# Performance work log

Measured on AMD Instinct MI355X. Metric: run time of the kernel, lower is better.

The kernel has to match this reference:

```python
import jax, jax.numpy as jnp
import numpy as np

N_NODES = 50000


def gin_conv(x, src, dst, W, b, eps=0.0):
    # GINConv: nn((1+eps)*x_i + sum_{j in N(i)} x_j)
    agg = jax.ops.segment_sum(x[src], dst, num_segments=N_NODES)  # [N, D]
    h = (1.0 + eps) * x + agg
    return h @ W + b


def setup_inputs() -> dict:
    key = jax.random.key(0)
    ks = jax.random.split(key, 8)
    n, e = N_NODES, 800000
    d_in, d_h, d_out = 128, 128, 64
    feature = jax.random.normal(ks[0], (n, d_in), dtype=jnp.float32)
    edge_index = jax.random.randint(ks[1], (2, e), 0, n, dtype=jnp.int64)
    s1 = 1.0 / np.sqrt(d_in)
    sh = 1.0 / np.sqrt(d_h)
    W1 = jax.random.normal(ks[2], (d_in, d_h), dtype=jnp.float32) * s1
    b1 = jnp.zeros((d_h,), dtype=jnp.float32)
    Wh = jax.random.normal(ks[3], (d_h, d_h), dtype=jnp.float32) * sh
    bh = jnp.zeros((d_h,), dtype=jnp.float32)
    Wo = jax.random.normal(ks[4], (d_h, d_out), dtype=jnp.float32) * sh
    bo = jnp.zeros((d_out,), dtype=jnp.float32)
    return {"feature": feature, "edge_index": edge_index, "W1": W1, "b1": b1,
            "Wh": Wh, "bh": bh, "Wo": Wo, "bo": bo}


def reference(feature, edge_index, W1, b1, Wh, bh, Wo, bo):
    src, dst = edge_index[0], edge_index[1]
    x = gin_conv(feature, src, dst, W1, b1)
    x = jax.nn.relu(x)
    # one hidden layer (layer_num=3); dropout disabled (eval)
    x = gin_conv(x, src, dst, Wh, bh)
    x = jax.nn.relu(x)
    x = gin_conv(x, src, dst, Wo, bo)
    return jax.nn.log_softmax(x, axis=1)
```

## Files before the change

### kernel.cpp

```cpp
#include <hip/hip_runtime.h>

typedef short short8 __attribute__((ext_vector_type(8)));
typedef float f32x4 __attribute__((ext_vector_type(4)));


__device__ inline unsigned short f2bf(float f) {
    union { float f; unsigned u; } v; v.f = f;
    unsigned r = v.u + 0x7fffu + ((v.u >> 16) & 1u);
    return (unsigned short)(r >> 16);
}
__device__ inline unsigned pack2(float a, float b) {
    return (unsigned)f2bf(a) | ((unsigned)f2bf(b) << 16);
}
__device__ inline float bflo(unsigned u) { union { unsigned q; float f; } c; c.q = u << 16; return c.f; }
__device__ inline float bfhi(unsigned u) { union { unsigned q; float f; } c; c.q = u & 0xffff0000u; return c.f; }


#define EPB 2048
#define NE 8
#define BSH 9
#define MAXBKT 128
#define DCAP 10240

__global__ __launch_bounds__(256) void binA(const int* __restrict__ src, const int* __restrict__ dst,
                                            int* __restrict__ cnt2d, int e, int nbkt, int nblk) {
    __shared__ int hist[MAXBKT];
    int t = threadIdx.x, blk = blockIdx.x;
    for (int b = t; b < nbkt; b += 256) hist[b] = 0;
    __syncthreads();
    int base = blk * EPB;
#pragma unroll
    for (int j = 0; j < NE; j++) {
        int idx = base + t + 256 * j;
        if (idx < e) atomicAdd(&hist[dst[idx] >> BSH], 1);
    }
    __syncthreads();
    for (int b = t; b < nbkt; b += 256) cnt2d[b * nblk + blk] = hist[b];
}

__global__ __launch_bounds__(512) void scanB1(int* __restrict__ cnt2d, int* __restrict__ totals, int nblk) {
    __shared__ int s[512];
    int t = threadIdx.x, b = blockIdx.x;
    int v = (t < nblk) ? cnt2d[b * nblk + t] : 0;
    s[t] = v;
    __syncthreads();
    for (int off = 1; off < 512; off <<= 1) {
        int u = (t >= off) ? s[t - off] : 0;
        __syncthreads();
        s[t] += u;
        __syncthreads();
    }
    if (t < nblk) cnt2d[b * nblk + t] = s[t] - v;
    if (t == nblk - 1) totals[b] = s[t];
}

__global__ __launch_bounds__(128) void scanB2(const int* __restrict__ totals, int* __restrict__ bbase,
                                              int* __restrict__ row_ptr, int nbkt, int n, int e) {
    __shared__ int s[128];
    int t = threadIdx.x;
    int v = (t < nbkt) ? totals[t] : 0;
    s[t] = v;
    __syncthreads();
    for (int off = 1; off < 128; off <<= 1) {
        int u = (t >= off) ? s[t - off] : 0;
        __syncthreads();
        s[t] += u;
        __syncthreads();
    }
    if (t < nbkt) bbase[t] = s[t] - v;
    if (t == 0) row_ptr[n] = e;
}

__global__ __launch_bounds__(256) void binC(const int* __restrict__ src, const int* __restrict__ dst,
                                            const int* __restrict__ cnt2d, const int* __restrict__ bbase,
                                            unsigned* __restrict__ pairs, int e, int nbkt, int nblk) {
    __shared__ int hist[MAXBKT], loff[MAXBKT], cur[MAXBKT], gb[MAXBKT];
    __shared__ int sc[256];
    __shared__ unsigned sorted[EPB];
    int t = threadIdx.x, blk = blockIdx.x;
    for (int b = t; b < nbkt; b += 256) hist[b] = 0;
    __syncthreads();
    int base = blk * EPB;
    int cnt = min(EPB, e - base);
    unsigned packed[NE];
    int bb[NE];
#pragma unroll
    for (int j = 0; j < NE; j++) {
        int idx = base + t + 256 * j;
        bb[j] = -1;
        if (idx < e) {
            unsigned s0 = (unsigned)src[idx], d = (unsigned)dst[idx];
            int b = (int)(d >> BSH);
            bb[j] = b;
            packed[j] = s0 | ((d & ((1u << BSH) - 1)) << 16) | ((unsigned)b << 25);
            atomicAdd(&hist[b], 1);
        }
    }
    __syncthreads();
    int v = (t < nbkt) ? hist[t] : 0;
    sc[t] = v;
    __syncthreads();
    for (int off = 1; off < 256; off <<= 1) {
        int u = (t >= off) ? sc[t - off] : 0;
        __syncthreads();
        sc[t] += u;
        __syncthreads();
    }
    if (t < nbkt) {
        int ex = sc[t] - v;
        loff[t] = ex;
        cur[t] = ex;
        gb[t] = bbase[t] + cnt2d[t * nblk + blk];
    }
    __syncthreads();
#pragma unroll
    for (int j = 0; j < NE; j++) {
        if (bb[j] >= 0) {
            int r = atomicAdd(&cur[bb[j]], 1);
            sorted[r] = packed[j];
        }
    }
    __syncthreads();
    for (int i = t; i < cnt; i += 256) {
        unsigned w = sorted[i];
        int b = (int)(w >> 25);
        pairs[gb[b] + (i - loff[b])] = w;
    }
}

__global__ __launch_bounds__(512) void buildD(const unsigned* __restrict__ pairs,
                                              const int* __restrict__ totals, const int* __restrict__ bbase,
                                              int* __restrict__ row_ptr, unsigned short* __restrict__ csr, int n) {
    __shared__ int hist[512], off[512];
    __shared__ unsigned short lcsr[DCAP];
    int t = threadIdx.x, b = blockIdx.x;
    int cnt = totals[b], base = bbase[b];
    hist[t] = 0;
    __syncthreads();
    for (int i = t; i < cnt; i += 512)
        atomicAdd(&hist[(pairs[base + i] >> 16) & 511], 1);
    __syncthreads();
    int v = hist[t];
    off[t] = v;
    __syncthreads();
    for (int o = 1; o < 512; o <<= 1) {
        int u = (t >= o) ? off[t - o] : 0;
        __syncthreads();
        off[t] += u;
        __syncthreads();
    }
    int excl = off[t] - v;
    int node = (b << BSH) + t;
    if (node < n) row_ptr[node] = base + excl;
    __syncthreads();
    hist[t] = excl;
    __syncthreads();
    for (int i = t; i < cnt; i += 512) {
        unsigned w = pairs[base + i];
        int r = atomicAdd(&hist[(w >> 16) & 511], 1);
        if (r < DCAP) lcsr[r] = (unsigned short)(w & 0xFFFFu);
    }
    __syncthreads();
    int lim = min(cnt, DCAP);
    for (int i = t; i < lim; i += 512) csr[base + i] = lcsr[i];
}


__global__ void cvt_bf16_kernel(const float4* __restrict__ in, uint2* __restrict__ out, int nf4) {
    int i = blockIdx.x * 256 + threadIdx.x;
    if (i < nf4) {
        float4 v = in[i];
        out[i] = make_uint2(pack2(v.x, v.y), pack2(v.z, v.w));
    }
}

__global__ void wt_all(const float* __restrict__ W1, const float* __restrict__ Wh, const float* __restrict__ Wo,
                       unsigned short* __restrict__ W1t, unsigned short* __restrict__ Wht,
                       unsigned short* __restrict__ Wot) {
    int i = blockIdx.x * 256 + threadIdx.x;
    if (i < 16384) {
        int k = i >> 7, nn = i & 127;
        W1t[nn * 128 + k] = f2bf(W1[i]);
    } else if (i < 32768) {
        int j = i - 16384, k = j >> 7, nn = j & 127;
        Wht[nn * 128 + k] = f2bf(Wh[j]);
    } else if (i < 40960) {
        int j = i - 32768, k = j >> 6, nn = j & 63;
        Wot[nn * 128 + k] = f2bf(Wo[j]);
    }
}


#define ACC8(vv)                                     \
    acc[0] += bflo(vv.x); acc[1] += bfhi(vv.x);      \
    acc[2] += bflo(vv.y); acc[3] += bfhi(vv.y);      \
    acc[4] += bflo(vv.z); acc[5] += bfhi(vv.z);      \
    acc[6] += bflo(vv.w); acc[7] += bfhi(vv.w);


template <bool SECOND>
__global__ __launch_bounds__(256) void fused_layer(
    const uint4* __restrict__ x, const int* __restrict__ row_ptr,
    const unsigned short* __restrict__ csr,
    const short8* __restrict__ Bt, const float* __restrict__ bias,
    unsigned short* __restrict__ out_h,
    const short8* __restrict__ Bt2,
    unsigned short* __restrict__ out_y,
    int n) {
    __shared__ unsigned short As[16][136];
    __shared__ unsigned short Hs[SECOND ? 16 : 1][SECOND ? 136 : 1];

    int t = threadIdx.x;
    int nl = t >> 4, chunk = t & 15;
    int r0 = blockIdx.x * 16;
    int node = r0 + nl;

    float acc[8] = {0.f, 0.f, 0.f, 0.f, 0.f, 0.f, 0.f, 0.f};
    if (node < n) {
        size_t base = (size_t)node * 16 + chunk;
        uint4 s0 = x[base];
        ACC8(s0)
        int beg = row_ptr[node], end = row_ptr[node + 1];
        int ed = beg;
        for (; ed + 8 <= end; ed += 8) {
            int idx[8];
#pragma unroll
            for (int j = 0; j < 8; j++) idx[j] = csr[ed + j];
            uint4 v[8];
#pragma unroll
            for (int j = 0; j < 8; j++) v[j] = x[(size_t)idx[j] * 16 + chunk];
#pragma unroll
            for (int j = 0; j < 8; j++) { ACC8(v[j]) }
        }
        for (; ed + 4 <= end; ed += 4) {
            int i0 = csr[ed], i1 = csr[ed + 1], i2 = csr[ed + 2], i3 = csr[ed + 3];
            uint4 v0 = x[(size_t)i0 * 16 + chunk];
            uint4 v1 = x[(size_t)i1 * 16 + chunk];
            uint4 v2 = x[(size_t)i2 * 16 + chunk];
            uint4 v3 = x[(size_t)i3 * 16 + chunk];
            ACC8(v0) ACC8(v1) ACC8(v2) ACC8(v3)
        }
        for (; ed < end; ++ed) {
            uint4 v0 = x[(size_t)csr[ed] * 16 + chunk];
            ACC8(v0)
        }
    }
    uint4 packed;
    packed.x = pack2(acc[0], acc[1]); packed.y = pack2(acc[2], acc[3]);
    packed.z = pack2(acc[4], acc[5]); packed.w = pack2(acc[6], acc[7]);
    ((uint4*)&As[nl][0])[chunk] = packed;
    __syncthreads();

    int wid = t >> 6, lane = t & 63;
    int lm = lane & 15, lq = lane >> 4;

    short8 a[4];
#pragma unroll
    for (int kc = 0; kc < 4; kc++)
        a[kc] = *(const short8*)&As[lm][kc * 32 + lq * 8];

    f32x4 hacc[2];
#pragma unroll
    for (int nt = 0; nt < 2; nt++) hacc[nt] = (f32x4){0.f, 0.f, 0.f, 0.f};
#pragma unroll
    for (int nt = 0; nt < 2; nt++) {
        int ct = wid * 2 + nt;
        const short8* Br = Bt + (size_t)(ct * 16 + lm) * 16;
#pragma unroll
        for (int kc = 0; kc < 4; kc++)
            hacc[nt] = __builtin_amdgcn_mfma_f32_16x16x32_bf16(a[kc], Br[kc * 4 + lq], hacc[nt], 0, 0, 0);
    }

#pragma unroll
    for (int nt = 0; nt < 2; nt++) {
        int col = (wid * 2 + nt) * 16 + lm;
        float bv = bias[col];
#pragma unroll
        for (int i = 0; i < 4; i++) {
            int row = r0 + lq * 4 + i;
            float v = fmaxf(hacc[nt][i] + bv, 0.f);
            if (SECOND) {
                Hs[lq * 4 + i][col] = f2bf(v);
            } else if (row < n) {
                out_h[(size_t)row * 128 + col] = f2bf(v);
            }
        }
    }

    if (SECOND) {
        __syncthreads();
        short8 a2[4];
#pragma unroll
        for (int kc = 0; kc < 4; kc++)
            a2[kc] = *(const short8*)&Hs[lm][kc * 32 + lq * 8];
        f32x4 yacc = (f32x4){0.f, 0.f, 0.f, 0.f};
        const short8* Br2 = Bt2 + (size_t)(wid * 16 + lm) * 16;
#pragma unroll
        for (int kc = 0; kc < 4; kc++)
            yacc = __builtin_amdgcn_mfma_f32_16x16x32_bf16(a2[kc], Br2[kc * 4 + lq], yacc, 0, 0, 0);
        int col = wid * 16 + lm;
#pragma unroll
        for (int i = 0; i < 4; i++) {
            int row = r0 + lq * 4 + i;
            if (row < n) out_y[(size_t)row * 64 + col] = f2bf(yacc[i]);
        }
    }
}


__global__ __launch_bounds__(256) void agg_lsm(
    const uint4* __restrict__ x, float* __restrict__ out,
    const int* __restrict__ row_ptr, const unsigned short* __restrict__ csr,
    const float* __restrict__ bo, int n) {
    int gt = blockIdx.x * 256 + threadIdx.x;
    int node = gt >> 3, lane = gt & 7;
    if (node >= n) return;
    size_t base = (size_t)node * 8 + lane;
    uint4 s0 = x[base];
    float acc[8] = { bflo(s0.x), bfhi(s0.x), bflo(s0.y), bfhi(s0.y),
                     bflo(s0.z), bfhi(s0.z), bflo(s0.w), bfhi(s0.w) };
    int beg = row_ptr[node], end = row_ptr[node + 1];
    int ed = beg;
    for (; ed + 8 <= end; ed += 8) {
        int idx[8];
#pragma unroll
        for (int j = 0; j < 8; j++) idx[j] = csr[ed + j];
        uint4 v[8];
#pragma unroll
        for (int j = 0; j < 8; j++) v[j] = x[(size_t)idx[j] * 8 + lane];
#pragma unroll
        for (int j = 0; j < 8; j++) { ACC8(v[j]) }
    }
    for (; ed + 4 <= end; ed += 4) {
        int i0 = csr[ed], i1 = csr[ed + 1], i2 = csr[ed + 2], i3 = csr[ed + 3];
        uint4 v0 = x[(size_t)i0 * 8 + lane];
        uint4 v1 = x[(size_t)i1 * 8 + lane];
        uint4 v2 = x[(size_t)i2 * 8 + lane];
        uint4 v3 = x[(size_t)i3 * 8 + lane];
        ACC8(v0) ACC8(v1) ACC8(v2) ACC8(v3)
    }
    for (; ed < end; ++ed) {
        uint4 v0 = x[(size_t)csr[ed] * 8 + lane];
        ACC8(v0)
    }
    const float4* bo4 = (const float4*)bo;
    float4 bA = bo4[lane * 2], bB = bo4[lane * 2 + 1];
    acc[0] += bA.x; acc[1] += bA.y; acc[2] += bA.z; acc[3] += bA.w;
    acc[4] += bB.x; acc[5] += bB.y; acc[6] += bB.z; acc[7] += bB.w;
    float m = acc[0];
#pragma unroll
    for (int j = 1; j < 8; j++) m = fmaxf(m, acc[j]);
#pragma unroll
    for (int off = 1; off < 8; off <<= 1) m = fmaxf(m, __shfl_xor(m, off, 64));
    float s = 0.f;
#pragma unroll
    for (int j = 0; j < 8; j++) s += __expf(acc[j] - m);
#pragma unroll
    for (int off = 1; off < 8; off <<= 1) s += __shfl_xor(s, off, 64);
    float ls = m + __logf(s);
    float4 o0 = make_float4(acc[0] - ls, acc[1] - ls, acc[2] - ls, acc[3] - ls);
    float4 o1 = make_float4(acc[4] - ls, acc[5] - ls, acc[6] - ls, acc[7] - ls);
    float4* op = (float4*)(out + (size_t)node * 64 + lane * 8);
    op[0] = o0;
    op[1] = o1;
}


extern "C" void kernel_launch(void* const* d_in, const int* in_sizes, int n_in,
                              void* d_out, int out_size, void* d_ws, size_t ws_size,
                              hipStream_t stream) {
    const float* feature = (const float*)d_in[0];
    const int*   edges   = (const int*)d_in[1];
    const float* W1 = (const float*)d_in[2];
    const float* b1 = (const float*)d_in[3];
    const float* Wh = (const float*)d_in[4];
    const float* bh = (const float*)d_in[5];
    const float* Wo = (const float*)d_in[6];
    const float* bo = (const float*)d_in[7];

    int n = in_sizes[0] / 128;
    int e = in_sizes[1] / 2;
    const int* src = edges;
    const int* dst = edges + e;

    int nbkt = (n + 511) >> BSH;
    int nblk = (e + EPB - 1) / EPB;

    char* ws = (char*)d_ws;
    auto take = [&](size_t bytes) {
        char* p = ws;
        ws += (bytes + 255) & ~(size_t)255;
        return p;
    };
    int* cnt2d   = (int*)take((size_t)nbkt * nblk * 4);
    int* totals  = (int*)take((size_t)nbkt * 4);
    int* bbase   = (int*)take((size_t)(nbkt + 1) * 4);
    int* row_ptr = (int*)take((size_t)(n + 1) * 4);
    unsigned* pairs = (unsigned*)take((size_t)e * 4);
    unsigned short* csr = (unsigned short*)take((size_t)e * 2);
    unsigned short* featb = (unsigned short*)take((size_t)n * 128 * 2);
    unsigned short* hb    = (unsigned short*)take((size_t)n * 128 * 2);
    unsigned short* yb    = (unsigned short*)take((size_t)n * 64 * 2);
    unsigned short* W1t = (unsigned short*)take(128 * 128 * 2);
    unsigned short* Wht = (unsigned short*)take(128 * 128 * 2);
    unsigned short* Wot = (unsigned short*)take(64 * 128 * 2);

    binA<<<nblk, 256, 0, stream>>>(src, dst, cnt2d, e, nbkt, nblk);
    scanB1<<<nbkt, 512, 0, stream>>>(cnt2d, totals, nblk);
    scanB2<<<1, 128, 0, stream>>>(totals, bbase, row_ptr, nbkt, n, e);
    binC<<<nblk, 256, 0, stream>>>(src, dst, cnt2d, bbase, pairs, e, nbkt, nblk);
    buildD<<<nbkt, 512, 0, stream>>>(pairs, totals, bbase, row_ptr, csr, n);

    cvt_bf16_kernel<<<(n * 32 + 255) / 256, 256, 0, stream>>>(
        (const float4*)feature, (uint2*)featb, n * 32);
    wt_all<<<160, 256, 0, stream>>>(W1, Wh, Wo, W1t, Wht, Wot);

    int fblocks = (n + 15) / 16;

    fused_layer<false><<<fblocks, 256, 0, stream>>>(
        (const uint4*)featb, row_ptr, csr, (const short8*)W1t, b1,
        hb, nullptr, nullptr, n);

    fused_layer<true><<<fblocks, 256, 0, stream>>>(
        (const uint4*)hb, row_ptr, csr, (const short8*)Wht, bh,
        nullptr, (const short8*)Wot, yb, n);

    agg_lsm<<<(n * 8 + 255) / 256, 256, 0, stream>>>(
        (const uint4*)yb, (float*)d_out, row_ptr, csr, bo, n);
}
```

Measured before the change: 221.1 us.

## Balance edge aggregation across block threads and merge preprocessing kernels

The gather-sum in fused_layer and agg_lsm now splits each block's contiguous CSR edge range evenly across thread slots rather than giving one node to each thread group. Partial sums are accumulated into fp32 shared memory with atomics, then converted to bf16 for the MFMA stage. This is meant to remove load imbalance from varying node degrees. The edge histogram, feature bf16 conversion and weight transpose are also merged into one launch to cut launch overhead. The cost is shared-memory atomics, a larger fp32 staging tile, and extra conversion work before the MFMAs.

```diff
diff --git a/kernel.cpp b/kernel.cpp
--- a/kernel.cpp
+++ b/kernel.cpp
@@ -14,6 +14,12 @@
 }
 __device__ inline float bflo(unsigned u) { union { unsigned q; float f; } c; c.q = u << 16; return c.f; }
 __device__ inline float bfhi(unsigned u) { union { unsigned q; float f; } c; c.q = u & 0xffff0000u; return c.f; }
+
+#define ACC8(vv)                                     \
+    acc[0] += bflo(vv.x); acc[1] += bfhi(vv.x);      \
+    acc[2] += bflo(vv.y); acc[3] += bfhi(vv.y);      \
+    acc[4] += bflo(vv.z); acc[5] += bfhi(vv.z);      \
+    acc[6] += bflo(vv.w); acc[7] += bfhi(vv.w);
 
 
 #define EPB 2048
@@ -22,20 +28,46 @@
 #define MAXBKT 128
 #define DCAP 10240
 
-__global__ __launch_bounds__(256) void binA(const int* __restrict__ src, const int* __restrict__ dst,
-                                            int* __restrict__ cnt2d, int e, int nbkt, int nblk) {
+__global__ __launch_bounds__(256) void mega1(const int* __restrict__ dst, int* __restrict__ cnt2d,
+                                             int e, int nbkt, int nblk,
+                                             const float4* __restrict__ feat, uint2* __restrict__ featb,
+                                             int cvtb, int nf4,
+                                             const float* __restrict__ W1, const float* __restrict__ Wh,
+                                             const float* __restrict__ Wo,
+                                             unsigned short* __restrict__ W1t, unsigned short* __restrict__ Wht,
+                                             unsigned short* __restrict__ Wot) {
     __shared__ int hist[MAXBKT];
-    int t = threadIdx.x, blk = blockIdx.x;
-    for (int b = t; b < nbkt; b += 256) hist[b] = 0;
-    __syncthreads();
-    int base = blk * EPB;
-#pragma unroll
-    for (int j = 0; j < NE; j++) {
-        int idx = base + t + 256 * j;
-        if (idx < e) atomicAdd(&hist[dst[idx] >> BSH], 1);
-    }
-    __syncthreads();
-    for (int b = t; b < nbkt; b += 256) cnt2d[b * nblk + blk] = hist[b];
+    int t = threadIdx.x, b = blockIdx.x;
+    if (b < nblk) {
+        for (int j = t; j < nbkt; j += 256) hist[j] = 0;
+        __syncthreads();
+        int base = b * EPB;
+#pragma unroll
+        for (int j = 0; j < NE; j++) {
+            int idx = base + t + 256 * j;
+            if (idx < e) atomicAdd(&hist[dst[idx] >> BSH], 1);
+        }
+        __syncthreads();
+        for (int j = t; j < nbkt; j += 256) cnt2d[j * nblk + b] = hist[j];
+    } else if (b < nblk + cvtb) {
+        int i = (b - nblk) * 256 + t;
+        if (i < nf4) {
+            float4 v = feat[i];
+            featb[i] = make_uint2(pack2(v.x, v.y), pack2(v.z, v.w));
+        }
+    } else {
+        int i = (b - nblk - cvtb) * 256 + t;
+        if (i < 16384) {
+            int k = i >> 7, nn = i & 127;
+            W1t[nn * 128 + k] = f2bf(W1[i]);
+        } else if (i < 32768) {
+            int j = i - 16384, k = j >> 7, nn = j & 127;
+            Wht[nn * 128 + k] = f2bf(Wh[j]);
+        } else if (i < 40960) {
+            int j = i - 32768, k = j >> 6, nn = j & 63;
+            Wot[nn * 128 + k] = f2bf(Wo[j]);
+        }
+    }
 }
 
 __global__ __launch_bounds__(512) void scanB1(int* __restrict__ cnt2d, int* __restrict__ totals, int nblk) {
@@ -166,38 +198,6 @@
 }
 
 
-__global__ void cvt_bf16_kernel(const float4* __restrict__ in, uint2* __restrict__ out, int nf4) {
-    int i = blockIdx.x * 256 + threadIdx.x;
-    if (i < nf4) {
-        float4 v = in[i];
-        out[i] = make_uint2(pack2(v.x, v.y), pack2(v.z, v.w));
-    }
-}
-
-__global__ void wt_all(const float* __restrict__ W1, const float* __restrict__ Wh, const float* __restrict__ Wo,
-                       unsigned short* __restrict__ W1t, unsigned short* __restrict__ Wht,
-                       unsigned short* __restrict__ Wot) {
-    int i = blockIdx.x * 256 + threadIdx.x;
-    if (i < 16384) {
-        int k = i >> 7, nn = i & 127;
-        W1t[nn * 128 + k] = f2bf(W1[i]);
-    } else if (i < 32768) {
-        int j = i - 16384, k = j >> 7, nn = j & 127;
-        Wht[nn * 128 + k] = f2bf(Wh[j]);
-    } else if (i < 40960) {
-        int j = i - 32768, k = j >> 6, nn = j & 63;
-        Wot[nn * 128 + k] = f2bf(Wo[j]);
-    }
-}
-
-
-#define ACC8(vv)                                     \
-    acc[0] += bflo(vv.x); acc[1] += bfhi(vv.x);      \
-    acc[2] += bflo(vv.y); acc[3] += bfhi(vv.y);      \
-    acc[4] += bflo(vv.z); acc[5] += bfhi(vv.z);      \
-    acc[6] += bflo(vv.w); acc[7] += bfhi(vv.w);
-
-
 template <bool SECOND>
 __global__ __launch_bounds__(256) void fused_layer(
     const uint4* __restrict__ x, const int* __restrict__ row_ptr,
@@ -207,48 +207,67 @@
     const short8* __restrict__ Bt2,
     unsigned short* __restrict__ out_y,
     int n) {
-    __shared__ unsigned short As[16][136];
+    __shared__ float Af[16][132];
+    __shared__ int rp[17];
     __shared__ unsigned short Hs[SECOND ? 16 : 1][SECOND ? 136 : 1];
 
     int t = threadIdx.x;
-    int nl = t >> 4, chunk = t & 15;
     int r0 = blockIdx.x * 16;
-    int node = r0 + nl;
-
-    float acc[8] = {0.f, 0.f, 0.f, 0.f, 0.f, 0.f, 0.f, 0.f};
-    if (node < n) {
-        size_t base = (size_t)node * 16 + chunk;
-        uint4 s0 = x[base];
-        ACC8(s0)
-        int beg = row_ptr[node], end = row_ptr[node + 1];
-        int ed = beg;
-        for (; ed + 8 <= end; ed += 8) {
-            int idx[8];
-#pragma unroll
-            for (int j = 0; j < 8; j++) idx[j] = csr[ed + j];
-            uint4 v[8];
-#pragma unroll
-            for (int j = 0; j < 8; j++) v[j] = x[(size_t)idx[j] * 16 + chunk];
-#pragma unroll
-            for (int j = 0; j < 8; j++) { ACC8(v[j]) }
-        }
-        for (; ed + 4 <= end; ed += 4) {
-            int i0 = csr[ed], i1 = csr[ed + 1], i2 = csr[ed + 2], i3 = csr[ed + 3];
-            uint4 v0 = x[(size_t)i0 * 16 + chunk];
-            uint4 v1 = x[(size_t)i1 * 16 + chunk];
-            uint4 v2 = x[(size_t)i2 * 16 + chunk];
-            uint4 v3 = x[(size_t)i3 * 16 + chunk];
-            ACC8(v0) ACC8(v1) ACC8(v2) ACC8(v3)
-        }
-        for (; ed < end; ++ed) {
-            uint4 v0 = x[(size_t)csr[ed] * 16 + chunk];
-            ACC8(v0)
-        }
-    }
-    uint4 packed;
-    packed.x = pack2(acc[0], acc[1]); packed.y = pack2(acc[2], acc[3]);
-    packed.z = pack2(acc[4], acc[5]); packed.w = pack2(acc[6], acc[7]);
-    ((uint4*)&As[nl][0])[chunk] = packed;
+    if (t < 17) rp[t] = row_ptr[min(r0 + t, n)];
+
+    {
+        int nl = t >> 4, chunk = t & 15;
+        int node = r0 + nl;
+        float acc[8] = {0.f, 0.f, 0.f, 0.f, 0.f, 0.f, 0.f, 0.f};
+        if (node < n) {
+            uint4 s0 = x[(size_t)node * 16 + chunk];
+            ACC8(s0)
+        }
+#pragma unroll
+        for (int j = 0; j < 8; j++) Af[nl][chunk * 8 + j] = acc[j];
+    }
+    __syncthreads();
+
+    {
+        int col = t & 15, slot = t >> 4;
+        int E0 = rp[0], E1 = rp[16];
+        int Eb = E1 - E0;
+        int per = (Eb + 15) >> 4;
+        int ed = E0 + slot * per;
+        int mye = min(ed + per, E1);
+        int nd = 0;
+        while (ed < mye) {
+            while (nd < 15 && rp[nd + 1] <= ed) nd++;
+            int stop = min(mye, rp[nd + 1]);
+            float acc[8] = {0.f, 0.f, 0.f, 0.f, 0.f, 0.f, 0.f, 0.f};
+            int k = ed;
+            for (; k + 8 <= stop; k += 8) {
+                int idx[8];
+#pragma unroll
+                for (int j = 0; j < 8; j++) idx[j] = csr[k + j];
+                uint4 v[8];
+#pragma unroll
+                for (int j = 0; j < 8; j++) v[j] = x[(size_t)idx[j] * 16 + col];
+#pragma unroll
+                for (int j = 0; j < 8; j++) { ACC8(v[j]) }
+            }
+            for (; k + 4 <= stop; k += 4) {
+                int i0 = csr[k], i1 = csr[k + 1], i2 = csr[k + 2], i3 = csr[k + 3];
+                uint4 v0 = x[(size_t)i0 * 16 + col];
+                uint4 v1 = x[(size_t)i1 * 16 + col];
+                uint4 v2 = x[(size_t)i2 * 16 + col];
+                uint4 v3 = x[(size_t)i3 * 16 + col];
+                ACC8(v0) ACC8(v1) ACC8(v2) ACC8(v3)
+            }
+            for (; k < stop; ++k) {
+                uint4 v0 = x[(size_t)csr[k] * 16 + col];
+                ACC8(v0)
+            }
+#pragma unroll
+            for (int j = 0; j < 8; j++) atomicAdd(&Af[nd][col * 8 + j], acc[j]);
+            ed = stop;
+        }
+    }
     __syncthreads();
 
     int wid = t >> 6, lane = t & 63;
@@ -256,16 +275,20 @@
 
     short8 a[4];
 #pragma unroll
-    for (int kc = 0; kc < 4; kc++)
-        a[kc] = *(const short8*)&As[lm][kc * 32 + lq * 8];
+    for (int kc = 0; kc < 4; kc++) {
+        const float* p = &Af[lm][kc * 32 + lq * 8];
+        short8 s;
+#pragma unroll
+        for (int j = 0; j < 8; j++) s[j] = (short)f2bf(p[j]);
+        a[kc] = s;
+    }
 
     f32x4 hacc[2];
 #pragma unroll
     for (int nt = 0; nt < 2; nt++) hacc[nt] = (f32x4){0.f, 0.f, 0.f, 0.f};
 #pragma unroll
     for (int nt = 0; nt < 2; nt++) {
-        int ct = wid * 2 + nt;
-        const short8* Br = Bt + (size_t)(ct * 16 + lm) * 16;
+        const short8* Br = Bt + (size_t)((wid * 2 + nt) * 16 + lm) * 16;
 #pragma unroll
         for (int kc = 0; kc < 4; kc++)
             hacc[nt] = __builtin_amdgcn_mfma_f32_16x16x32_bf16(a[kc], Br[kc * 4 + lq], hacc[nt], 0, 0, 0);
@@ -312,39 +335,66 @@
     const uint4* __restrict__ x, float* __restrict__ out,
     const int* __restrict__ row_ptr, const unsigned short* __restrict__ csr,
     const float* __restrict__ bo, int n) {
-    int gt = blockIdx.x * 256 + threadIdx.x;
-    int node = gt >> 3, lane = gt & 7;
+    __shared__ float Af[32][68];
+    __shared__ int rp[33];
+
+    int t = threadIdx.x;
+    int r0 = blockIdx.x * 32;
+    if (t < 33) rp[t] = row_ptr[min(r0 + t, n)];
+
+    {
+        int nl = t >> 3, chunk = t & 7;
+        int node = r0 + nl;
+        float acc[8] = {0.f, 0.f, 0.f, 0.f, 0.f, 0.f, 0.f, 0.f};
+        if (node < n) {
+            uint4 s0 = x[(size_t)node * 8 + chunk];
+            ACC8(s0)
+        }
+#pragma unroll
+        for (int j = 0; j < 8; j++) Af[nl][chunk * 8 + j] = acc[j];
+    }
+    __syncthreads();
+
+    {
+        int col = t & 7, slot = t >> 3;
+        int E0 = rp[0], E1 = rp[32];
+        int Eb = E1 - E0;
+        int per = (Eb + 31) >> 5;
+        int ed = E0 + slot * per;
+        int mye = min(ed + per, E1);
+        int nd = 0;
+        while (ed < mye) {
+            while (nd < 31 && rp[nd + 1] <= ed) nd++;
+            int stop = min(mye, rp[nd + 1]);
+            float acc[8] = {0.f, 0.f, 0.f, 0.f, 0.f, 0.f, 0.f, 0.f};
+            int k = ed;
+            for (; k + 4 <= stop; k += 4) {
+                int i0 = csr[k], i1 = csr[k + 1], i2 = csr[k + 2], i3 = csr[k + 3];
+                uint4 v0 = x[(size_t)i0 * 8 + col];
+                uint4 v1 = x[(size_t)i1 * 8 + col];
+                uint4 v2 = x[(size_t)i2 * 8 + col];
+                uint4 v3 = x[(size_t)i3 * 8 + col];
+                ACC8(v0) ACC8(v1) ACC8(v2) ACC8(v3)
+            }
+            for (; k < stop; ++k) {
+                uint4 v0 = x[(size_t)csr[k] * 8 + col];
+                ACC8(v0)
+            }
+#pragma unroll
+            for (int j = 0; j < 8; j++) atomicAdd(&Af[nd][col * 8 + j], acc[j]);
+            ed = stop;
+        }
+    }
+    __syncthreads();
+
+    int nl = t >> 3, col = t & 7;
+    int node = r0 + nl;
     if (node >= n) return;
-    size_t base = (size_t)node * 8 + lane;
-    uint4 s0 = x[base];
-    float acc[8] = { bflo(s0.x), bfhi(s0.x), bflo(s0.y), bfhi(s0.y),
-                     bflo(s0.z), bfhi(s0.z), bflo(s0.w), bfhi(s0.w) };
-    int beg = row_ptr[node], end = row_ptr[node + 1];
-    int ed = beg;
-    for (; ed + 8 <= end; ed += 8) {
-        int idx[8];
-#pragma unroll
-        for (int j = 0; j < 8; j++) idx[j] = csr[ed + j];
-        uint4 v[8];
-#pragma unroll
-        for (int j = 0; j < 8; j++) v[j] = x[(size_t)idx[j] * 8 + lane];
-#pragma unroll
-        for (int j = 0; j < 8; j++) { ACC8(v[j]) }
-    }
-    for (; ed + 4 <= end; ed += 4) {
-        int i0 = csr[ed], i1 = csr[ed + 1], i2 = csr[ed + 2], i3 = csr[ed + 3];
-        uint4 v0 = x[(size_t)i0 * 8 + lane];
-        uint4 v1 = x[(size_t)i1 * 8 + lane];
-        uint4 v2 = x[(size_t)i2 * 8 + lane];
-        uint4 v3 = x[(size_t)i3 * 8 + lane];
-        ACC8(v0) ACC8(v1) ACC8(v2) ACC8(v3)
-    }
-    for (; ed < end; ++ed) {
-        uint4 v0 = x[(size_t)csr[ed] * 8 + lane];
-        ACC8(v0)
-    }
+    float acc[8];
+#pragma unroll
+    for (int j = 0; j < 8; j++) acc[j] = Af[nl][col * 8 + j];
     const float4* bo4 = (const float4*)bo;
-    float4 bA = bo4[lane * 2], bB = bo4[lane * 2 + 1];
+    float4 bA = bo4[col * 2], bB = bo4[col * 2 + 1];
     acc[0] += bA.x; acc[1] += bA.y; acc[2] += bA.z; acc[3] += bA.w;
     acc[4] += bB.x; acc[5] += bB.y; acc[6] += bB.z; acc[7] += bB.w;
     float m = acc[0];
@@ -360,7 +410,7 @@
     float ls = m + __logf(s);
     float4 o0 = make_float4(acc[0] - ls, acc[1] - ls, acc[2] - ls, acc[3] - ls);
     float4 o1 = make_float4(acc[4] - ls, acc[5] - ls, acc[6] - ls, acc[7] - ls);
-    float4* op = (float4*)(out + (size_t)node * 64 + lane * 8);
+    float4* op = (float4*)(out + (size_t)node * 64 + col * 8);
     op[0] = o0;
     op[1] = o1;
 }
@@ -385,6 +435,8 @@
 
     int nbkt = (n + 511) >> BSH;
     int nblk = (e + EPB - 1) / EPB;
+    int nf4 = n * 32;
+    int cvtb = (nf4 + 255) / 256;
 
     char* ws = (char*)d_ws;
     auto take = [&](size_t bytes) {
@@ -405,16 +457,15 @@
     unsigned short* Wht = (unsigned short*)take(128 * 128 * 2);
     unsigned short* Wot = (unsigned short*)take(64 * 128 * 2);
 
-    binA<<<nblk, 256, 0, stream>>>(src, dst, cnt2d, e, nbkt, nblk);
+    mega1<<<nblk + cvtb + 160, 256, 0, stream>>>(
+        dst, cnt2d, e, nbkt, nblk,
+        (const float4*)feature, (uint2*)featb, cvtb, nf4,
+        W1, Wh, Wo, W1t, Wht, Wot);
     scanB1<<<nbkt, 512, 0, stream>>>(cnt2d, totals, nblk);
     scanB2<<<1, 128, 0, stream>>>(totals, bbase, row_ptr, nbkt, n, e);
     binC<<<nblk, 256, 0, stream>>>(src, dst, cnt2d, bbase, pairs, e, nbkt, nblk);
     buildD<<<nbkt, 512, 0, stream>>>(pairs, totals, bbase, row_ptr, csr, n);
 
-    cvt_bf16_kernel<<<(n * 32 + 255) / 256, 256, 0, stream>>>(
-        (const float4*)feature, (uint2*)featb, n * 32);
-    wt_all<<<160, 256, 0, stream>>>(W1, Wh, Wo, W1t, Wht, Wot);
-
     int fblocks = (n + 15) / 16;
 
     fused_layer<false><<<fblocks, 256, 0, stream>>>(
@@ -425,6 +476,6 @@
         (const uint4*)hb, row_ptr, csr, (const short8*)Wht, bh,
         nullptr, (const short8*)Wot, yb, n);
 
-    agg_lsm<<<(n * 8 + 255) / 256, 256, 0, stream>>>(
+    agg_lsm<<<(n + 31) / 32, 256, 0, stream>>>(
         (const uint4*)yb, (float*)d_out, row_ptr, csr, bo, n);
 }
```

After: 337.1 us. 52.5% more time.

## Merge prep kernels into one launch and stage block CSR slices in LDS

Applied to the files above, without the earlier changes.

The histogram, feature bf16 conversion and weight transpose kernels are combined into a single launch by splitting on block index, which removes two launches. The fused layer and final aggregation kernels now load each block's contiguous CSR neighbour indices into shared memory cooperatively before the gather. Each thread then reads indices from LDS rather than issuing scattered small global loads, with a fallback to global reads when the slice exceeds the cap. This costs an extra barrier and some LDS per block.

```diff
diff --git a/kernel.cpp b/kernel.cpp
--- a/kernel.cpp
+++ b/kernel.cpp
@@ -14,6 +14,40 @@
 }
 __device__ inline float bflo(unsigned u) { union { unsigned q; float f; } c; c.q = u << 16; return c.f; }
 __device__ inline float bfhi(unsigned u) { union { unsigned q; float f; } c; c.q = u & 0xffff0000u; return c.f; }
+
+#define ACC8(vv)                                     \
+    acc[0] += bflo(vv.x); acc[1] += bfhi(vv.x);      \
+    acc[2] += bflo(vv.y); acc[3] += bfhi(vv.y);      \
+    acc[4] += bflo(vv.z); acc[5] += bfhi(vv.z);      \
+    acc[6] += bflo(vv.w); acc[7] += bfhi(vv.w);
+
+template <int TPN, typename F>
+__device__ __forceinline__ void gather_acc(float acc[8], const uint4* __restrict__ x,
+                                           int lane, int beg, int end, F geti) {
+    int k = beg;
+    for (; k + 8 <= end; k += 8) {
+        int idx[8];
+#pragma unroll
+        for (int j = 0; j < 8; j++) idx[j] = geti(k + j);
+        uint4 v[8];
+#pragma unroll
+        for (int j = 0; j < 8; j++) v[j] = x[(size_t)idx[j] * TPN + lane];
+#pragma unroll
+        for (int j = 0; j < 8; j++) { ACC8(v[j]) }
+    }
+    for (; k + 4 <= end; k += 4) {
+        int i0 = geti(k), i1 = geti(k + 1), i2 = geti(k + 2), i3 = geti(k + 3);
+        uint4 v0 = x[(size_t)i0 * TPN + lane];
+        uint4 v1 = x[(size_t)i1 * TPN + lane];
+        uint4 v2 = x[(size_t)i2 * TPN + lane];
+        uint4 v3 = x[(size_t)i3 * TPN + lane];
+        ACC8(v0) ACC8(v1) ACC8(v2) ACC8(v3)
+    }
+    for (; k < end; ++k) {
+        uint4 v0 = x[(size_t)geti(k) * TPN + lane];
+        ACC8(v0)
+    }
+}
 
 
 #define EPB 2048
@@ -22,20 +56,46 @@
 #define MAXBKT 128
 #define DCAP 10240
 
-__global__ __launch_bounds__(256) void binA(const int* __restrict__ src, const int* __restrict__ dst,
-                                            int* __restrict__ cnt2d, int e, int nbkt, int nblk) {
+__global__ __launch_bounds__(256) void mega1(const int* __restrict__ dst, int* __restrict__ cnt2d,
+                                             int e, int nbkt, int nblk,
+                                             const float4* __restrict__ feat, uint2* __restrict__ featb,
+                                             int cvtb, int nf4,
+                                             const float* __restrict__ W1, const float* __restrict__ Wh,
+                                             const float* __restrict__ Wo,
+                                             unsigned short* __restrict__ W1t, unsigned short* __restrict__ Wht,
+                                             unsigned short* __restrict__ Wot) {
     __shared__ int hist[MAXBKT];
-    int t = threadIdx.x, blk = blockIdx.x;
-    for (int b = t; b < nbkt; b += 256) hist[b] = 0;
-    __syncthreads();
-    int base = blk * EPB;
-#pragma unroll
-    for (int j = 0; j < NE; j++) {
-        int idx = base + t + 256 * j;
-        if (idx < e) atomicAdd(&hist[dst[idx] >> BSH], 1);
-    }
-    __syncthreads();
-    for (int b = t; b < nbkt; b += 256) cnt2d[b * nblk + blk] = hist[b];
+    int t = threadIdx.x, b = blockIdx.x;
+    if (b < nblk) {
+        for (int j = t; j < nbkt; j += 256) hist[j] = 0;
+        __syncthreads();
+        int base = b * EPB;
+#pragma unroll
+        for (int j = 0; j < NE; j++) {
+            int idx = base + t + 256 * j;
+            if (idx < e) atomicAdd(&hist[dst[idx] >> BSH], 1);
+        }
+        __syncthreads();
+        for (int j = t; j < nbkt; j += 256) cnt2d[j * nblk + b] = hist[j];
+    } else if (b < nblk + cvtb) {
+        int i = (b - nblk) * 256 + t;
+        if (i < nf4) {
+            float4 v = feat[i];
+            featb[i] = make_uint2(pack2(v.x, v.y), pack2(v.z, v.w));
+        }
+    } else {
+        int i = (b - nblk - cvtb) * 256 + t;
+        if (i < 16384) {
+            int k = i >> 7, nn = i & 127;
+            W1t[nn * 128 + k] = f2bf(W1[i]);
+        } else if (i < 32768) {
+            int j = i - 16384, k = j >> 7, nn = j & 127;
+            Wht[nn * 128 + k] = f2bf(Wh[j]);
+        } else if (i < 40960) {
+            int j = i - 32768, k = j >> 6, nn = j & 63;
+            Wot[nn * 128 + k] = f2bf(Wo[j]);
+        }
+    }
 }
 
 __global__ __launch_bounds__(512) void scanB1(int* __restrict__ cnt2d, int* __restrict__ totals, int nblk) {
@@ -166,37 +226,7 @@
 }
 
 
-__global__ void cvt_bf16_kernel(const float4* __restrict__ in, uint2* __restrict__ out, int nf4) {
-    int i = blockIdx.x * 256 + threadIdx.x;
-    if (i < nf4) {
-        float4 v = in[i];
-        out[i] = make_uint2(pack2(v.x, v.y), pack2(v.z, v.w));
-    }
-}
-
-__global__ void wt_all(const float* __restrict__ W1, const float* __restrict__ Wh, const float* __restrict__ Wo,
-                       unsigned short* __restrict__ W1t, unsigned short* __restrict__ Wht,
-                       unsigned short* __restrict__ Wot) {
-    int i = blockIdx.x * 256 + threadIdx.x;
-    if (i < 16384) {
-        int k = i >> 7, nn = i & 127;
-        W1t[nn * 128 + k] = f2bf(W1[i]);
-    } else if (i < 32768) {
-        int j = i - 16384, k = j >> 7, nn = j & 127;
-        Wht[nn * 128 + k] = f2bf(Wh[j]);
-    } else if (i < 40960) {
-        int j = i - 32768, k = j >> 6, nn = j & 63;
-        Wot[nn * 128 + k] = f2bf(Wo[j]);
-    }
-}
-
-
-#define ACC8(vv)                                     \
-    acc[0] += bflo(vv.x); acc[1] += bfhi(vv.x);      \
-    acc[2] += bflo(vv.y); acc[3] += bfhi(vv.y);      \
-    acc[4] += bflo(vv.z); acc[5] += bfhi(vv.z);      \
-    acc[6] += bflo(vv.w); acc[7] += bfhi(vv.w);
-
+#define ECAP 1024
 
 template <bool SECOND>
 __global__ __launch_bounds__(256) void fused_layer(
@@ -209,40 +239,30 @@
     int n) {
     __shared__ unsigned short As[16][136];
     __shared__ unsigned short Hs[SECOND ? 16 : 1][SECOND ? 136 : 1];
+    __shared__ unsigned short eidx[ECAP];
 
     int t = threadIdx.x;
     int nl = t >> 4, chunk = t & 15;
     int r0 = blockIdx.x * 16;
     int node = r0 + nl;
 
+    int E0 = row_ptr[r0 < n ? r0 : n];
+    int E1 = row_ptr[min(r0 + 16, n)];
+    int ecnt = min(E1 - E0, ECAP);
+    for (int i = t; i < ecnt; i += 256) eidx[i] = csr[E0 + i];
+    __syncthreads();
+
     float acc[8] = {0.f, 0.f, 0.f, 0.f, 0.f, 0.f, 0.f, 0.f};
     if (node < n) {
-        size_t base = (size_t)node * 16 + chunk;
-        uint4 s0 = x[base];
+        uint4 s0 = x[(size_t)node * 16 + chunk];
         ACC8(s0)
         int beg = row_ptr[node], end = row_ptr[node + 1];
-        int ed = beg;
-        for (; ed + 8 <= end; ed += 8) {
-            int idx[8];
-#pragma unroll
-            for (int j = 0; j < 8; j++) idx[j] = csr[ed + j];
-            uint4 v[8];
-#pragma unroll
-            for (int j = 0; j < 8; j++) v[j] = x[(size_t)idx[j] * 16 + chunk];
-#pragma unroll
-            for (int j = 0; j < 8; j++) { ACC8(v[j]) }
-        }
-        for (; ed + 4 <= end; ed += 4) {
-            int i0 = csr[ed], i1 = csr[ed + 1], i2 = csr[ed + 2], i3 = csr[ed + 3];
-            uint4 v0 = x[(size_t)i0 * 16 + chunk];
-            uint4 v1 = x[(size_t)i1 * 16 + chunk];
-            uint4 v2 = x[(size_t)i2 * 16 + chunk];
-            uint4 v3 = x[(size_t)i3 * 16 + chunk];
-            ACC8(v0) ACC8(v1) ACC8(v2) ACC8(v3)
-        }
-        for (; ed < end; ++ed) {
-            uint4 v0 = x[(size_t)csr[ed] * 16 + chunk];
-            ACC8(v0)
+        if (end - E0 <= ECAP) {
+            gather_acc<16>(acc, x, chunk, beg - E0, end - E0,
+                           [&](int k) { return (int)eidx[k]; });
+        } else {
+            gather_acc<16>(acc, x, chunk, beg, end,
+                           [&](int k) { return (int)csr[k]; });
         }
     }
     uint4 packed;
@@ -264,8 +284,7 @@
     for (int nt = 0; nt < 2; nt++) hacc[nt] = (f32x4){0.f, 0.f, 0.f, 0.f};
 #pragma unroll
     for (int nt = 0; nt < 2; nt++) {
-        int ct = wid * 2 + nt;
-        const short8* Br = Bt + (size_t)(ct * 16 + lm) * 16;
+        const short8* Br = Bt + (size_t)((wid * 2 + nt) * 16 + lm) * 16;
 #pragma unroll
         for (int kc = 0; kc < 4; kc++)
             hacc[nt] = __builtin_amdgcn_mfma_f32_16x16x32_bf16(a[kc], Br[kc * 4 + lq], hacc[nt], 0, 0, 0);
@@ -308,41 +327,36 @@
 }
 
 
+#define ECAP2 1536
+
 __global__ __launch_bounds__(256) void agg_lsm(
     const uint4* __restrict__ x, float* __restrict__ out,
     const int* __restrict__ row_ptr, const unsigned short* __restrict__ csr,
     const float* __restrict__ bo, int n) {
-    int gt = blockIdx.x * 256 + threadIdx.x;
-    int node = gt >> 3, lane = gt & 7;
+    __shared__ unsigned short eidx[ECAP2];
+    int t = threadIdx.x;
+    int r0 = blockIdx.x * 32;
+    int node = r0 + (t >> 3), lane = t & 7;
+
+    int E0 = row_ptr[r0 < n ? r0 : n];
+    int E1 = row_ptr[min(r0 + 32, n)];
+    int ecnt = min(E1 - E0, ECAP2);
+    for (int i = t; i < ecnt; i += 256) eidx[i] = csr[E0 + i];
+    __syncthreads();
+
     if (node >= n) return;
-    size_t base = (size_t)node * 8 + lane;
-    uint4 s0 = x[base];
+    uint4 s0 = x[(size_t)node * 8 + lane];
     float acc[8] = { bflo(s0.x), bfhi(s0.x), bflo(s0.y), bfhi(s0.y),
                      bflo(s0.z), bfhi(s0.z), bflo(s0.w), bfhi(s0.w) };
     int beg = row_ptr[node], end = row_ptr[node + 1];
-    int ed = beg;
-    for (; ed + 8 <= end; ed += 8) {
-        int idx[8];
-#pragma unroll
-        for (int j = 0; j < 8; j++) idx[j] = csr[ed + j];
-        uint4 v[8];
-#pragma unroll
-        for (int j = 0; j < 8; j++) v[j] = x[(size_t)idx[j] * 8 + lane];
-#pragma unroll
-        for (int j = 0; j < 8; j++) { ACC8(v[j]) }
-    }
-    for (; ed + 4 <= end; ed += 4) {
-        int i0 = csr[ed], i1 = csr[ed + 1], i2 = csr[ed + 2], i3 = csr[ed + 3];
-        uint4 v0 = x[(size_t)i0 * 8 + lane];
-        uint4 v1 = x[(size_t)i1 * 8 + lane];
-        uint4 v2 = x[(size_t)i2 * 8 + lane];
-        uint4 v3 = x[(size_t)i3 * 8 + lane];
-        ACC8(v0) ACC8(v1) ACC8(v2) ACC8(v3)
-    }
-    for (; ed < end; ++ed) {
-        uint4 v0 = x[(size_t)csr[ed] * 8 + lane];
-        ACC8(v0)
-    }
+    if (end - E0 <= ECAP2) {
+        gather_acc<8>(acc, x, lane, beg - E0, end - E0,
+                      [&](int k) { return (int)eidx[k]; });
+    } else {
+        gather_acc<8>(acc, x, lane, beg, end,
+                      [&](int k) { return (int)csr[k]; });
+    }
+
     const float4* bo4 = (const float4*)bo;
     float4 bA = bo4[lane * 2], bB = bo4[lane * 2 + 1];
     acc[0] += bA.x; acc[1] += bA.y; acc[2] += bA.z; acc[3] += bA.w;
@@ -385,6 +399,8 @@
 
     int nbkt = (n + 511) >> BSH;
     int nblk = (e + EPB - 1) / EPB;
+    int nf4 = n * 32;
+    int cvtb = (nf4 + 255) / 256;
 
     char* ws = (char*)d_ws;
     auto take = [&](size_t bytes) {
@@ -405,16 +421,15 @@
     unsigned short* Wht = (unsigned short*)take(128 * 128 * 2);
     unsigned short* Wot = (unsigned short*)take(64 * 128 * 2);
 
-    binA<<<nblk, 256, 0, stream>>>(src, dst, cnt2d, e, nbkt, nblk);
+    mega1<<<nblk + cvtb + 160, 256, 0, stream>>>(
+        dst, cnt2d, e, nbkt, nblk,
+        (const float4*)feature, (uint2*)featb, cvtb, nf4,
+        W1, Wh, Wo, W1t, Wht, Wot);
     scanB1<<<nbkt, 512, 0, stream>>>(cnt2d, totals, nblk);
     scanB2<<<1, 128, 0, stream>>>(totals, bbase, row_ptr, nbkt, n, e);
     binC<<<nblk, 256, 0, stream>>>(src, dst, cnt2d, bbase, pairs, e, nbkt, nblk);
     buildD<<<nbkt, 512, 0, stream>>>(pairs, totals, bbase, row_ptr, csr, n);
 
-    cvt_bf16_kernel<<<(n * 32 + 255) / 256, 256, 0, stream>>>(
-        (const float4*)feature, (uint2*)featb, n * 32);
-    wt_all<<<160, 256, 0, stream>>>(W1, Wh, Wo, W1t, Wht, Wot);
-
     int fblocks = (n + 15) / 16;
 
     fused_layer<false><<<fblocks, 256, 0, stream>>>(
@@ -425,6 +440,6 @@
         (const uint4*)hb, row_ptr, csr, (const short8*)Wht, bh,
         nullptr, (const short8*)Wot, yb, n);
 
-    agg_lsm<<<(n * 8 + 255) / 256, 256, 0, stream>>>(
+    agg_lsm<<<(n + 31) / 32, 256, 0, stream>>>(
         (const uint4*)yb, (float*)d_out, row_ptr, csr, bo, n);
 }
```

Result: faster. 208.9 us (-5.5%).
